# Kernel tuning notes

Hardware: AMD Instinct MI355X
Metric: run time of the kernel (lower is better)

The kernel has to match this reference:

```python
import jax, jax.numpy as jnp
import numpy as np

TAIL = 10.0
K = 8
MIN_W = 1e-3
MIN_H = 1e-3
MIN_D = 1e-3
EPS = 1e-12
D_ID = 32   # identity dims
D_TR = 32   # transformed dims
HID = 256


def setup_inputs() -> dict:
    key = jax.random.key(0)
    k0, k1, k2, k3, k4 = jax.random.split(key, 5)
    B = 131072
    inputs = jax.random.normal(k0, (B, D_ID + D_TR), dtype=jnp.float32)
    W1 = jax.random.normal(k1, (D_ID, HID), dtype=jnp.float32) * (1.0 / np.sqrt(D_ID))
    b1 = jnp.zeros((HID,), dtype=jnp.float32)
    W2 = jax.random.normal(k2, (HID, D_TR * (3 * K + 1)), dtype=jnp.float32) * (1.0 / np.sqrt(HID))
    b2 = jnp.zeros((D_TR * (3 * K + 1),), dtype=jnp.float32)
    return {"inputs": inputs, "W1": W1, "b1": b1, "W2": W2, "b2": b2}


def _normalize_bin_params(un_w, un_h, un_d):
    # widths
    w = jax.nn.softmax(un_w, axis=-1)
    w = MIN_W + (1.0 - MIN_W * K) * w
    cw = jnp.cumsum(w, axis=-1)
    cw = jnp.pad(cw, [(0, 0)] * (cw.ndim - 1) + [(1, 0)])
    cw = cw / jnp.clip(cw[..., -1:], 1e-12)
    w = cw[..., 1:] - cw[..., :-1]
    # heights
    h = jax.nn.softmax(un_h, axis=-1)
    h = MIN_H + (1.0 - MIN_H * K) * h
    ch = jnp.cumsum(h, axis=-1)
    ch = jnp.pad(ch, [(0, 0)] * (ch.ndim - 1) + [(1, 0)])
    ch = ch / jnp.clip(ch[..., -1:], 1e-12)
    h = ch[..., 1:] - ch[..., :-1]
    d = MIN_D + jax.nn.softplus(un_d)
    return w, cw, h, ch, d


def _rqs_forward(x, w, cw, h, ch, d):
    # x: (N,); bins: (N,K) / (N,K+1). Linear tails outside [-TAIL, TAIL].
    inside = (x >= -TAIL) & (x <= TAIL)
    xs = jnp.clip((x + TAIL) / (2.0 * TAIL), 0.0, 1.0)
    bin_ids = jnp.clip(jnp.sum(xs[:, None] >= cw, axis=-1) - 1, 0, K - 1)
    take = lambda t, idx: jnp.take_along_axis(t, idx[:, None], axis=-1)[:, 0]
    xk = take(cw, bin_ids)
    wk = take(w, bin_ids)
    yk = take(ch, bin_ids)
    hk = take(h, bin_ids)
    dk = take(d, bin_ids)
    dk1 = take(d, bin_ids + 1)
    t = jnp.clip((xs - xk) / (wk + EPS), 0.0, 1.0)
    a = (hk + EPS) / (wk + EPS)
    b = dk
    c = dk1
    num = a * t * t + b * t * (1.0 - t)
    den = a + (b + c - 2.0 * a) * t * (1.0 - t)
    s = num / (den + EPS)
    ys = yk + hk * s
    y = ys * (2.0 * TAIL) - TAIL
    deriv_num = a * a * (c * t * t + 2.0 * a * t * (1.0 - t) + b * (1.0 - t) * (1.0 - t))
    dydx = deriv_num / (den * den + EPS)  # (top-bottom)/(right-left) == 1
    lad = jnp.log(jnp.clip(dydx, 1e-12))
    return jnp.where(inside, y, x), jnp.where(inside, lad, 0.0)


def reference(inputs, W1, b1, W2, b2):
    identity = inputs[:, :D_ID]          # mask <= 0 columns
    to_transform = inputs[:, D_ID:]      # mask > 0 columns
    Bsz = inputs.shape[0]
    params = jax.nn.relu(identity @ W1 + b1) @ W2 + b2
    p = params.reshape(Bsz, D_TR, 3 * K + 1)
    un_w, un_h, un_d = p[..., :K], p[..., K:2 * K], p[..., 2 * K:]
    w, cw, h, ch, d = _normalize_bin_params(un_w, un_h, un_d)
    # flatten (Bsz, D_TR, ...) -> (Bsz*D_TR, ...)
    xf = to_transform.reshape(-1)
    yf, ladf = _rqs_forward(
        xf,
        w.reshape(-1, K), cw.reshape(-1, K + 1),
        h.reshape(-1, K), ch.reshape(-1, K + 1),
        d.reshape(-1, K + 1),
    )
    outputs = jnp.concatenate([identity, yf.reshape(Bsz, D_TR)], axis=1)
    logabsdet = ladf.reshape(Bsz, D_TR).sum(axis=1)
    return outputs, logabsdet
```

## Files before the change

kernel.cpp:

```cpp
#include <hip/hip_runtime.h>
#include <math.h>

#define NROWS 131072
#define HID 256
#define NPAR 800
#define MROWS 64
#define NTHREADS 1024
#define NBLOCKS (NROWS / MROWS)

#define W2F_FRAGS 25600
#define LDS_HLO 32768
#define LDS_X   65536
#define LDS_TOTAL 102528

typedef __attribute__((ext_vector_type(8))) short s16x8;
typedef __attribute__((ext_vector_type(4))) float f32x4;

__device__ __forceinline__ unsigned short bf16_rne(float f) {
    unsigned u = __float_as_uint(f);
    u += 0x7fffu + ((u >> 16) & 1u);
    return (unsigned short)(u >> 16);
}

__global__ void prep_w2(const float* __restrict__ W2, short* __restrict__ wsp)
{
    const int t = blockIdx.x * 256 + threadIdx.x;
    if (t >= W2F_FRAGS) return;
    const int l = t & 63;
    const int g = t >> 6;
    const int ct = g >> 3, k0 = g & 7;
    const int c  = (ct << 4) + (l & 15);
    const int kb = (k0 << 5) + ((l >> 4) << 3);
    s16x8 hi, lo;
#pragma unroll
    for (int j = 0; j < 8; ++j) {
        float v = W2[(size_t)(kb + j) * NPAR + c];
        unsigned short h = bf16_rne(v);
        float hf = __uint_as_float((unsigned)h << 16);
        unsigned short lw = bf16_rne(v - hf);
        hi[j] = (short)h;
        lo[j] = (short)lw;
    }
    ((s16x8*)wsp)[g * 128 + l * 2]     = hi;
    ((s16x8*)wsp)[g * 128 + l * 2 + 1] = lo;
}

__global__ __launch_bounds__(NTHREADS, 4)
void rqs_fused(const float* __restrict__ inp,
               const float* __restrict__ W1,
               const float* __restrict__ b1,
               const short* __restrict__ W2F,
               const float* __restrict__ b2,
               float* __restrict__ out)
{
    extern __shared__ char smem[];
    char*  hhi   = smem;
    char*  hlo   = smem + LDS_HLO;
    float* x_lds = (float*)(smem + LDS_X);
    float* p_lds = (float*)smem;

    const int t    = threadIdx.x;
    const int row0 = blockIdx.x * MROWS;
    const int lane = t & 63;
    const int w    = t >> 6;
    const int arow = lane & 15;
    const int kgrp = lane >> 4;
    const int lane2 = lane << 1;

    const s16x8* BF = (const s16x8*)W2F;

    const int nct = (w < 2) ? 4 : 3;

    if (t < 512) {
        const int r = t >> 3, q = t & 7;
        const float4 v = ((const float4*)(inp + (size_t)(row0 + r) * 64))[q];
        ((float4*)(out + (size_t)(row0 + r) * 64))[q] = v;
        ((float4*)(x_lds + r * 32))[q] = v;
    }
    __syncthreads();

    {
        const int j = t & 255;
        const int q = t >> 8;
        float w1v[32];
#pragma unroll
        for (int k = 0; k < 32; ++k) w1v[k] = W1[k * HID + j];
        const float bj = b1[j];
        for (int rr = 0; rr < 16; ++rr) {
            const int r = q * 16 + rr;
            const float4* xr = (const float4*)(x_lds + r * 32);
            float s0 = bj, s1 = 0.f, s2 = 0.f, s3 = 0.f;
#pragma unroll
            for (int qq = 0; qq < 8; ++qq) {
                const float4 xv = xr[qq];
                s0 = fmaf(xv.x, w1v[4 * qq + 0], s0);
                s1 = fmaf(xv.y, w1v[4 * qq + 1], s1);
                s2 = fmaf(xv.z, w1v[4 * qq + 2], s2);
                s3 = fmaf(xv.w, w1v[4 * qq + 3], s3);
            }
            const float s = fmaxf((s0 + s1) + (s2 + s3), 0.0f);
            unsigned short hs = bf16_rne(s);
            float hf = __uint_as_float((unsigned)hs << 16);
            unsigned short ls = bf16_rne(s - hf);
            int byte = (r << 9) + (j << 1);
            byte ^= (r & 7) << 4;
            *(short*)(hhi + byte) = (short)hs;
            *(short*)(hlo + byte) = (short)ls;
        }
    }
    __syncthreads();

    f32x4 acc[4][4];
#pragma unroll
    for (int ci = 0; ci < 4; ++ci)
#pragma unroll
        for (int rt = 0; rt < 4; ++rt)
            acc[ci][rt] = (f32x4){0.f, 0.f, 0.f, 0.f};

#pragma unroll 1
    for (int k0 = 0; k0 < 8; ++k0) {
        s16x8 ahi[4], alo[4];
#pragma unroll
        for (int rt = 0; rt < 4; ++rt) {
            const int row = rt * 16 + arow;
            int byte = (row << 9) + (k0 << 6) + (kgrp << 4);
            byte ^= (row & 7) << 4;
            ahi[rt] = *(const s16x8*)(hhi + byte);
            alo[rt] = *(const s16x8*)(hlo + byte);
        }
#pragma unroll
        for (int ci = 0; ci < 4; ++ci) {
            if (ci < nct) {
                const int ct = w + (ci << 4);
                const int f  = (ct * 8 + k0) * 128 + lane2;
                const s16x8 bh = BF[f];
                const s16x8 bl = BF[f + 1];
#pragma unroll
                for (int rt = 0; rt < 4; ++rt) {
                    acc[ci][rt] = __builtin_amdgcn_mfma_f32_16x16x32_bf16(ahi[rt], bh, acc[ci][rt], 0, 0, 0);
                    acc[ci][rt] = __builtin_amdgcn_mfma_f32_16x16x32_bf16(ahi[rt], bl, acc[ci][rt], 0, 0, 0);
                    acc[ci][rt] = __builtin_amdgcn_mfma_f32_16x16x32_bf16(alo[rt], bh, acc[ci][rt], 0, 0, 0);
                }
            }
        }
    }

    float lad_total = 0.0f;

#pragma unroll
    for (int rhalf = 0; rhalf < 2; ++rhalf) {
        __syncthreads();
#pragma unroll
        for (int ci = 0; ci < 4; ++ci) {
            if (ci < nct) {
                const int ct = w + (ci << 4);
                const float bias = b2[(ct << 4) + arow];
                const int col = (ct << 4) + arow;
#pragma unroll
                for (int rr = 0; rr < 2; ++rr) {
                    const int rt = rhalf * 2 + rr;
                    const f32x4 v = acc[ci][rt];
                    const int rowl = (rr << 4) + (kgrp << 2);
                    p_lds[(rowl + 0) * 801 + col] = v[0] + bias;
                    p_lds[(rowl + 1) * 801 + col] = v[1] + bias;
                    p_lds[(rowl + 2) * 801 + col] = v[2] + bias;
                    p_lds[(rowl + 3) * 801 + col] = v[3] + bias;
                }
            }
        }
        __syncthreads();

        {
            const int r_l = t >> 5;
            const int dl  = t & 31;
            const float* p = &p_lds[r_l * 801 + dl * 25];
            float pv[25];
#pragma unroll
            for (int j = 0; j < 25; ++j) pv[j] = p[j];

            float cw[9], ch[9], dd[9];
            {
                float mw = pv[0];
#pragma unroll
                for (int j = 1; j < 8; ++j) mw = fmaxf(mw, pv[j]);
                float e[8], sw = 0.f;
#pragma unroll
                for (int j = 0; j < 8; ++j) { e[j] = __expf(pv[j] - mw); sw += e[j]; }
                const float scale = 0.992f / sw;
                float run = 0.f;
                cw[0] = 0.f;
#pragma unroll
                for (int j = 0; j < 8; ++j) { run += 0.001f + e[j] * scale; cw[j + 1] = run; }
                const float icn = 1.0f / fmaxf(cw[8], 1e-12f);
#pragma unroll
                for (int j = 1; j <= 8; ++j) cw[j] *= icn;
            }
            {
                float mh = pv[8];
#pragma unroll
                for (int j = 1; j < 8; ++j) mh = fmaxf(mh, pv[8 + j]);
                float e[8], sh = 0.f;
#pragma unroll
                for (int j = 0; j < 8; ++j) { e[j] = __expf(pv[8 + j] - mh); sh += e[j]; }
                const float scale = 0.992f / sh;
                float run = 0.f;
                ch[0] = 0.f;
#pragma unroll
                for (int j = 0; j < 8; ++j) { run += 0.001f + e[j] * scale; ch[j + 1] = run; }
                const float icn = 1.0f / fmaxf(ch[8], 1e-12f);
#pragma unroll
                for (int j = 1; j <= 8; ++j) ch[j] *= icn;
            }
#pragma unroll
            for (int j = 0; j < 9; ++j) {
                const float u = pv[16 + j];
                dd[j] = 0.001f + fmaxf(u, 0.f) + __logf(1.0f + __expf(-fabsf(u)));
            }

            const int grow = row0 + rhalf * 32 + r_l;
            const float x = inp[(size_t)grow * 64 + 32 + dl];
            const float xs = fminf(fmaxf((x + 10.0f) * 0.05f, 0.f), 1.f);
            int b = 0;
#pragma unroll
            for (int j = 1; j <= 8; ++j) b += (xs >= cw[j]) ? 1 : 0;
            b = min(b, 7);

            float xk = 0.f, wk = 0.f, yk = 0.f, hk = 0.f, dk = 0.f, dk1 = 0.f;
#pragma unroll
            for (int j = 0; j < 8; ++j) {
                if (b == j) {
                    xk = cw[j]; wk = cw[j + 1] - cw[j];
                    yk = ch[j]; hk = ch[j + 1] - ch[j];
                    dk = dd[j]; dk1 = dd[j + 1];
                }
            }

            const float EPSf = 1e-12f;
            const float tt = fminf(fmaxf((xs - xk) / (wk + EPSf), 0.f), 1.f);
            const float a = (hk + EPSf) / (wk + EPSf);
            const float omt = 1.f - tt;
            const float tomt = tt * omt;
            const float num = a * tt * tt + dk * tomt;
            const float den = a + (dk + dk1 - 2.f * a) * tomt;
            const float sres = num / (den + EPSf);
            const float ys = yk + hk * sres;
            float y = ys * 20.0f - 10.0f;
            const float dnum = a * a * (dk1 * tt * tt + 2.f * a * tomt + dk * omt * omt);
            const float dydx = dnum / (den * den + EPSf);
            float lad = __logf(fmaxf(dydx, 1e-12f));

            const bool inside = (x >= -10.0f) && (x <= 10.0f);
            if (!inside) { y = x; lad = 0.0f; }

            out[(size_t)grow * 64 + 32 + dl] = y;

            float s = lad;
            s += __shfl_xor(s, 1, 64);
            s += __shfl_xor(s, 2, 64);
            s += __shfl_xor(s, 4, 64);
            s += __shfl_xor(s, 8, 64);
            s += __shfl_xor(s, 16, 64);
            if ((lane & 31) == 0) out[(size_t)NROWS * 64 + grow] = s;
            lad_total += s;
        }
    }
    (void)lad_total;
}

extern "C" void kernel_launch(void* const* d_in, const int* in_sizes, int n_in,
                              void* d_out, int out_size, void* d_ws, size_t ws_size,
                              hipStream_t stream) {
    const float* inp = (const float*)d_in[0];
    const float* W1  = (const float*)d_in[1];
    const float* b1  = (const float*)d_in[2];
    const float* W2  = (const float*)d_in[3];
    const float* b2  = (const float*)d_in[4];
    float* out = (float*)d_out;
    short* wsp = (short*)d_ws;

    static bool attr_done = false;
    if (!attr_done) {
        hipFuncSetAttribute((const void*)rqs_fused,
                            hipFuncAttributeMaxDynamicSharedMemorySize, LDS_TOTAL);
        attr_done = true;
    }

    hipLaunchKernelGGL(prep_w2, dim3(100), dim3(256), 0, stream, W2, wsp);
    hipLaunchKernelGGL(rqs_fused, dim3(NBLOCKS), dim3(NTHREADS), LDS_TOTAL, stream,
                       inp, W1, b1, (const short*)wsp, b2, out);
}
```

Measured before the change: 304.5 us.

## Halve rows per block and rebalance MFMA column tiles across waves

Each block now handles 32 rows with 512 threads instead of 64 rows with 1024 threads. Each wave now owns 6–7 column tiles over 2 row tiles instead of 3–4 over 4 row tiles. The LDS footprint roughly halves (the p_lds row stride is padded to 804), so more blocks can be resident per CU, and the shared-memory attribute call is dropped. s_setprio raises wave priority around the MFMA chains. In exchange, each W2 fragment is reused across fewer rows, and W1 is reloaded by twice as many blocks, which raises L2 traffic.

New measurement: 297.7 us. 2.2% less time.

```diff
diff --git a/kernel.cpp b/kernel.cpp
--- a/kernel.cpp
+++ b/kernel.cpp
@@ -4,14 +4,15 @@
 #define NROWS 131072
 #define HID 256
 #define NPAR 800
-#define MROWS 64
-#define NTHREADS 1024
+#define MROWS 32
+#define NTHREADS 512
 #define NBLOCKS (NROWS / MROWS)
 
 #define W2F_FRAGS 25600
-#define LDS_HLO 32768
-#define LDS_X   65536
-#define LDS_TOTAL 102528
+#define LDS_HLO 16384
+#define LDS_X   32768
+#define LDS_PLD 804
+#define LDS_TOTAL (16 * LDS_PLD * 4)
 
 typedef __attribute__((ext_vector_type(8))) short s16x8;
 typedef __attribute__((ext_vector_type(4))) float f32x4;
@@ -69,9 +70,9 @@
 
     const s16x8* BF = (const s16x8*)W2F;
 
-    const int nct = (w < 2) ? 4 : 3;
-
-    if (t < 512) {
+    const int nct = (w < 2) ? 7 : 6;
+
+    if (t < 256) {
         const int r = t >> 3, q = t & 7;
         const float4 v = ((const float4*)(inp + (size_t)(row0 + r) * 64))[q];
         ((float4*)(out + (size_t)(row0 + r) * 64))[q] = v;
@@ -110,18 +111,18 @@
     }
     __syncthreads();
 
-    f32x4 acc[4][4];
-#pragma unroll
-    for (int ci = 0; ci < 4; ++ci)
-#pragma unroll
-        for (int rt = 0; rt < 4; ++rt)
-            acc[ci][rt] = (f32x4){0.f, 0.f, 0.f, 0.f};
+    f32x4 acc[7][2];
+#pragma unroll
+    for (int ci = 0; ci < 7; ++ci) {
+        acc[ci][0] = (f32x4){0.f, 0.f, 0.f, 0.f};
+        acc[ci][1] = (f32x4){0.f, 0.f, 0.f, 0.f};
+    }
 
 #pragma unroll 1
     for (int k0 = 0; k0 < 8; ++k0) {
-        s16x8 ahi[4], alo[4];
-#pragma unroll
-        for (int rt = 0; rt < 4; ++rt) {
+        s16x8 ahi[2], alo[2];
+#pragma unroll
+        for (int rt = 0; rt < 2; ++rt) {
             const int row = rt * 16 + arow;
             int byte = (row << 9) + (k0 << 6) + (kgrp << 4);
             byte ^= (row & 7) << 4;
@@ -129,43 +130,39 @@
             alo[rt] = *(const s16x8*)(hlo + byte);
         }
 #pragma unroll
-        for (int ci = 0; ci < 4; ++ci) {
+        for (int ci = 0; ci < 7; ++ci) {
             if (ci < nct) {
-                const int ct = w + (ci << 4);
+                const int ct = w + (ci << 3);
                 const int f  = (ct * 8 + k0) * 128 + lane2;
                 const s16x8 bh = BF[f];
                 const s16x8 bl = BF[f + 1];
-#pragma unroll
-                for (int rt = 0; rt < 4; ++rt) {
-                    acc[ci][rt] = __builtin_amdgcn_mfma_f32_16x16x32_bf16(ahi[rt], bh, acc[ci][rt], 0, 0, 0);
-                    acc[ci][rt] = __builtin_amdgcn_mfma_f32_16x16x32_bf16(ahi[rt], bl, acc[ci][rt], 0, 0, 0);
-                    acc[ci][rt] = __builtin_amdgcn_mfma_f32_16x16x32_bf16(alo[rt], bh, acc[ci][rt], 0, 0, 0);
-                }
-            }
-        }
-    }
-
-    float lad_total = 0.0f;
+                __builtin_amdgcn_s_setprio(1);
+                acc[ci][0] = __builtin_amdgcn_mfma_f32_16x16x32_bf16(ahi[0], bh, acc[ci][0], 0, 0, 0);
+                acc[ci][1] = __builtin_amdgcn_mfma_f32_16x16x32_bf16(ahi[1], bh, acc[ci][1], 0, 0, 0);
+                acc[ci][0] = __builtin_amdgcn_mfma_f32_16x16x32_bf16(ahi[0], bl, acc[ci][0], 0, 0, 0);
+                acc[ci][1] = __builtin_amdgcn_mfma_f32_16x16x32_bf16(ahi[1], bl, acc[ci][1], 0, 0, 0);
+                acc[ci][0] = __builtin_amdgcn_mfma_f32_16x16x32_bf16(alo[0], bh, acc[ci][0], 0, 0, 0);
+                acc[ci][1] = __builtin_amdgcn_mfma_f32_16x16x32_bf16(alo[1], bh, acc[ci][1], 0, 0, 0);
+                __builtin_amdgcn_s_setprio(0);
+            }
+        }
+    }
 
 #pragma unroll
     for (int rhalf = 0; rhalf < 2; ++rhalf) {
         __syncthreads();
 #pragma unroll
-        for (int ci = 0; ci < 4; ++ci) {
+        for (int ci = 0; ci < 7; ++ci) {
             if (ci < nct) {
-                const int ct = w + (ci << 4);
+                const int ct = w + (ci << 3);
                 const float bias = b2[(ct << 4) + arow];
                 const int col = (ct << 4) + arow;
-#pragma unroll
-                for (int rr = 0; rr < 2; ++rr) {
-                    const int rt = rhalf * 2 + rr;
-                    const f32x4 v = acc[ci][rt];
-                    const int rowl = (rr << 4) + (kgrp << 2);
-                    p_lds[(rowl + 0) * 801 + col] = v[0] + bias;
-                    p_lds[(rowl + 1) * 801 + col] = v[1] + bias;
-                    p_lds[(rowl + 2) * 801 + col] = v[2] + bias;
-                    p_lds[(rowl + 3) * 801 + col] = v[3] + bias;
-                }
+                const f32x4 v = acc[ci][rhalf];
+                const int rowl = kgrp << 2;
+                p_lds[(rowl + 0) * LDS_PLD + col] = v[0] + bias;
+                p_lds[(rowl + 1) * LDS_PLD + col] = v[1] + bias;
+                p_lds[(rowl + 2) * LDS_PLD + col] = v[2] + bias;
+                p_lds[(rowl + 3) * LDS_PLD + col] = v[3] + bias;
             }
         }
         __syncthreads();
@@ -173,7 +170,7 @@
         {
             const int r_l = t >> 5;
             const int dl  = t & 31;
-            const float* p = &p_lds[r_l * 801 + dl * 25];
+            const float* p = &p_lds[r_l * LDS_PLD + dl * 25];
             float pv[25];
 #pragma unroll
             for (int j = 0; j < 25; ++j) pv[j] = p[j];
@@ -217,7 +214,7 @@
                 dd[j] = 0.001f + fmaxf(u, 0.f) + __logf(1.0f + __expf(-fabsf(u)));
             }
 
-            const int grow = row0 + rhalf * 32 + r_l;
+            const int grow = row0 + rhalf * 16 + r_l;
             const float x = inp[(size_t)grow * 64 + 32 + dl];
             const float xs = fminf(fmaxf((x + 10.0f) * 0.05f, 0.f), 1.f);
             int b = 0;
@@ -261,10 +258,8 @@
             s += __shfl_xor(s, 8, 64);
             s += __shfl_xor(s, 16, 64);
             if ((lane & 31) == 0) out[(size_t)NROWS * 64 + grow] = s;
-            lad_total += s;
-        }
-    }
-    (void)lad_total;
+        }
+    }
 }
 
 extern "C" void kernel_launch(void* const* d_in, const int* in_sizes, int n_in,
@@ -278,13 +273,6 @@
     float* out = (float*)d_out;
     short* wsp = (short*)d_ws;
 
-    static bool attr_done = false;
-    if (!attr_done) {
-        hipFuncSetAttribute((const void*)rqs_fused,
-                            hipFuncAttributeMaxDynamicSharedMemorySize, LDS_TOTAL);
-        attr_done = true;
-    }
-
     hipLaunchKernelGGL(prep_w2, dim3(100), dim3(256), 0, stream, W2, wsp);
     hipLaunchKernelGGL(rqs_fused, dim3(NBLOCKS), dim3(NTHREADS), LDS_TOTAL, stream,
                        inp, W1, b1, (const short*)wsp, b2, out);
```
